# Kernel tuning notes

Measured on AMD Instinct MI355X. Metric: run time of the kernel, lower is better.

## Reference

```python
import jax, jax.numpy as jnp
import numpy as np

B, S, D, H, DK, DV = 4, 1024, 1024, 16, 64, 64
NEG = jnp.float32(-1e10)


def setup_inputs() -> dict:
    key = jax.random.key(0)
    ks = jax.random.split(key, 9)
    q = jax.random.normal(ks[0], (B, S, D), dtype=jnp.float32)
    k = jax.random.normal(ks[1], (B, S, D), dtype=jnp.float32)
    v = jax.random.normal(ks[2], (B, S, D), dtype=jnp.float32)
    pad_mask_1 = jax.random.randint(ks[3], (B,), 1, S + 1, dtype=jnp.int32)
    pad_mask_2 = jax.random.randint(ks[4], (B,), 1, S + 1, dtype=jnp.int32)
    # Per-head projection weights stacked over heads (torch Linear, bias=False).
    sc = 1.0 / np.sqrt(D)
    Wq = jax.random.uniform(ks[5], (H, D, DK), jnp.float32, -sc, sc)
    Wk = jax.random.uniform(ks[6], (H, D, DK), jnp.float32, -sc, sc)
    Wv = jax.random.uniform(ks[7], (H, D, DV), jnp.float32, -sc, sc)
    Wo = jax.random.uniform(ks[8], (H * DV, D), jnp.float32, -sc, sc)
    return {"q": q, "k": k, "v": v, "pad_mask_1": pad_mask_1,
            "pad_mask_2": pad_mask_2, "Wq": Wq, "Wk": Wk, "Wv": Wv, "Wo": Wo}


def reference(q, k, v, pad_mask_1, pad_mask_2, Wq, Wk, Wv, Wo):
    Bq, Sq, _ = q.shape
    scale = jnp.sqrt(jnp.float32(Wq.shape[-1]))
    qh = jnp.einsum('bsd,hdk->bhsk', q, Wq)   # [B,H,S,DK]
    kh = jnp.einsum('bsd,hdk->bhsk', k, Wk)
    vh = jnp.einsum('bsd,hdv->bhsv', v, Wv)
    w = jnp.einsum('bhqk,bhtk->bhqt', qh, kh) / scale  # [B,H,S,S]
    idx = jnp.arange(Sq)
    # pad_mask_1: mask key columns >= length; pad_mask_2: mask query rows >= length
    key_dead = idx[None, :] >= pad_mask_1[:, None]      # [B,S]
    row_dead = idx[None, :] >= pad_mask_2[:, None]      # [B,S]
    w = jnp.where(key_dead[:, None, None, :], NEG, w)
    w = jnp.where(row_dead[:, None, :, None], NEG, w)
    # causal: w.tril() + (-1e10).triu(1) == keep lower triangle, NEG strictly above
    causal = idx[None, :] > idx[:, None]                # [S,S] strictly upper
    w = jnp.where(causal[None, None], NEG, w)
    a = jax.nn.softmax(w, axis=-1)
    o = jnp.einsum('bhqt,bhtv->bhqv', a, vh)            # [B,H,S,DV]
    o = o.transpose(0, 2, 1, 3).reshape(Bq, Sq, -1)     # concat heads (head-major)
    return o @ Wo
```

## Files before the change

kernel.cpp:

```cpp
#include <hip/hip_runtime.h>

#define B_ 4
#define S_ 1024
#define D_ 1024
#define H_ 16
#define BSD (B_*S_*D_)

typedef unsigned short ushort_t;
typedef __attribute__((ext_vector_type(8))) __bf16 bf16x8;
typedef __attribute__((ext_vector_type(8))) ushort_t ushortx8;
typedef __attribute__((ext_vector_type(4))) float f32x4;

__device__ __forceinline__ ushort_t f2bf(float f) {
  union { float f; unsigned int u; } x; x.f = f;
  unsigned int r = x.u + 0x7fffu + ((x.u >> 16) & 1u);
  return (ushort_t)(r >> 16);
}

__device__ __forceinline__ void gll16(const void* g, void* l) {
  __builtin_amdgcn_global_load_lds(
      (const __attribute__((address_space(1))) unsigned int*)g,
      (__attribute__((address_space(3))) unsigned int*)l, 16, 0, 0);
}

__global__ __launch_bounds__(256) void transpose_w(
    const float* __restrict__ Wq, const float* __restrict__ Wk,
    const float* __restrict__ Wv, const float* __restrict__ Wo,
    ushort_t* __restrict__ WqT, ushort_t* __restrict__ WkT,
    ushort_t* __restrict__ WvT, ushort_t* __restrict__ WoT)
{
  __shared__ float tile[64][65];
  int blk = blockIdx.x;
  const float* src; ushort_t* dst;
  size_t sbase, dbase; int ld_src, ld_dst, r0, c0;
  if (blk < 768) {
    int tz = blk / 256;
    int rem = blk % 256; int head = rem >> 4; int kt = rem & 15;
    src = (tz == 0) ? Wq : (tz == 1) ? Wk : Wv;
    dst = (tz == 0) ? WqT : (tz == 1) ? WkT : WvT;
    sbase = (size_t)head * 1024 * 64; dbase = (size_t)head * 64 * 1024;
    ld_src = 64; ld_dst = 1024; r0 = kt * 64; c0 = 0;
  } else {
    int idx = blk - 768; src = Wo; dst = WoT;
    sbase = 0; dbase = 0; ld_src = 1024; ld_dst = 1024;
    r0 = (idx >> 4) * 64; c0 = (idx & 15) * 64;
  }
  int tid = threadIdx.x; int col = tid & 63; int rbase = tid >> 6;
  #pragma unroll
  for (int j = 0; j < 16; ++j) {
    int row = j * 4 + rbase;
    tile[row][col] = src[sbase + (size_t)(r0 + row) * ld_src + c0 + col];
  }
  __syncthreads();
  #pragma unroll
  for (int j = 0; j < 16; ++j) {
    int orow = j * 4 + rbase;
    dst[dbase + (size_t)(c0 + orow) * ld_dst + r0 + col] = f2bf(tile[col][orow]);
  }
}

__device__ __forceinline__ void gemm_body_f32A(
    const float* __restrict__ Af, const ushort_t* __restrict__ BT,
    ushort_t* __restrict__ Cb, int epi, int m0, int n0, int K)
{
  __shared__ __align__(16) ushort_t As[2][128 * 64];
  __shared__ __align__(16) ushort_t Bs[2][128 * 64];
  const int tid = threadIdx.x;
  const int wave = tid >> 6, lane = tid & 63;
  const int wm = wave >> 2, wn = wave & 3;

  f32x4 acc[4][2] = {};
  float4 areg[2][2];

  auto loadA = [&](int k0) {
    #pragma unroll
    for (int i = 0; i < 2; ++i) {
      int off = ((i * 8 + wave) << 10) + lane * 16;
      int row = off >> 7;
      int cb = off & 127;
      int lcb = cb ^ ((row & 7) << 4);
      const float* src = Af + (size_t)(m0 + row) * K + k0 + (lcb >> 1);
      areg[i][0] = *(const float4*)(src);
      areg[i][1] = *(const float4*)(src + 4);
    }
  };
  auto writeA = [&](int buf) {
    #pragma unroll
    for (int i = 0; i < 2; ++i) {
      int off = ((i * 8 + wave) << 10) + lane * 16;
      ushortx8 t;
      #pragma unroll
      for (int j = 0; j < 4; ++j) {
        t[j]     = f2bf(((const float*)&areg[i][0])[j]);
        t[4 + j] = f2bf(((const float*)&areg[i][1])[j]);
      }
      *(ushortx8*)((char*)As[buf] + off) = t;
    }
  };
  auto stageB = [&](int buf, int k0) {
    #pragma unroll
    for (int i = 0; i < 2; ++i) {
      int off = ((i * 8 + wave) << 10) + lane * 16;
      int row = off >> 7;
      int cb = off & 127;
      int lcb = cb ^ ((row & 7) << 4);
      gll16(BT + (size_t)(n0 + row) * K + k0 + (lcb >> 1), (char*)Bs[buf] + off);
    }
  };

  auto compute = [&](int buf) {
    #pragma unroll
    for (int kk = 0; kk < 2; ++kk) {
      bf16x8 af[4], bfr[2];
      #pragma unroll
      for (int mf = 0; mf < 4; ++mf) {
        int row = wm * 64 + mf * 16 + (lane & 15);
        int cb = kk * 64 + ((lane >> 4) << 4);
        af[mf] = *(const bf16x8*)((const char*)As[buf] + (row << 7) + (cb ^ ((row & 7) << 4)));
      }
      #pragma unroll
      for (int nf = 0; nf < 2; ++nf) {
        int row = wn * 32 + nf * 16 + (lane & 15);
        int cb = kk * 64 + ((lane >> 4) << 4);
        bfr[nf] = *(const bf16x8*)((const char*)Bs[buf] + (row << 7) + (cb ^ ((row & 7) << 4)));
      }
      #pragma unroll
      for (int mf = 0; mf < 4; ++mf)
        #pragma unroll
        for (int nf = 0; nf < 2; ++nf)
          acc[mf][nf] = __builtin_amdgcn_mfma_f32_16x16x32_bf16(af[mf], bfr[nf], acc[mf][nf], 0, 0, 0);
    }
  };

  const int nt = K >> 6;
  loadA(0);
  stageB(0, 0);
  writeA(0);
  __syncthreads();
  int cur = 0;
  for (int t = 0; t < nt - 1; ++t) {
    loadA((t + 1) << 6);
    stageB(cur ^ 1, (t + 1) << 6);
    compute(cur);
    writeA(cur ^ 1);
    __syncthreads();
    cur ^= 1;
  }
  compute(cur);

  #pragma unroll
  for (int mf = 0; mf < 4; ++mf) {
    #pragma unroll
    for (int nf = 0; nf < 2; ++nf) {
      #pragma unroll
      for (int r = 0; r < 4; ++r) {
        int m = m0 + wm * 64 + mf * 16 + ((lane >> 4) << 2) + r;
        int n = n0 + wn * 32 + nf * 16 + (lane & 15);
        float val = acc[mf][nf][r];
        if (epi == 0) {
          int b = m >> 10, s = m & 1023, h = n >> 6, dk = n & 63;
          Cb[((((size_t)(b * H_ + h)) << 10) + s) * 64 + dk] = f2bf(val);
        } else {
          int b = m >> 10, s = m & 1023, h = n >> 6, dv = n & 63;
          Cb[((((size_t)(b * H_ + h)) * 64 + dv) << 10) + s] = f2bf(val);
        }
      }
    }
  }
}

__device__ __forceinline__ void gemm_body(
    const ushort_t* __restrict__ A, const ushort_t* __restrict__ BT,
    float* __restrict__ Cf, int m0, int n0, int K)
{
  __shared__ __align__(16) ushort_t As[2][128 * 64];
  __shared__ __align__(16) ushort_t Bs[2][128 * 64];
  const int tid = threadIdx.x;
  const int wave = tid >> 6, lane = tid & 63;
  const int wm = wave >> 2, wn = wave & 3;

  f32x4 acc[4][2] = {};

  auto stage = [&](int buf, int k0) {
    #pragma unroll
    for (int i = 0; i < 2; ++i) {
      int off = ((i * 8 + wave) << 10) + lane * 16;
      int row = off >> 7;
      int cb = off & 127;
      int lcb = cb ^ ((row & 7) << 4);
      gll16(A + (size_t)(m0 + row) * K + k0 + (lcb >> 1), (char*)As[buf] + off);
      gll16(BT + (size_t)(n0 + row) * K + k0 + (lcb >> 1), (char*)Bs[buf] + off);
    }
  };

  auto compute = [&](int buf) {
    #pragma unroll
    for (int kk = 0; kk < 2; ++kk) {
      bf16x8 af[4], bfr[2];
      #pragma unroll
      for (int mf = 0; mf < 4; ++mf) {
        int row = wm * 64 + mf * 16 + (lane & 15);
        int cb = kk * 64 + ((lane >> 4) << 4);
        af[mf] = *(const bf16x8*)((const char*)As[buf] + (row << 7) + (cb ^ ((row & 7) << 4)));
      }
      #pragma unroll
      for (int nf = 0; nf < 2; ++nf) {
        int row = wn * 32 + nf * 16 + (lane & 15);
        int cb = kk * 64 + ((lane >> 4) << 4);
        bfr[nf] = *(const bf16x8*)((const char*)Bs[buf] + (row << 7) + (cb ^ ((row & 7) << 4)));
      }
      #pragma unroll
      for (int mf = 0; mf < 4; ++mf)
        #pragma unroll
        for (int nf = 0; nf < 2; ++nf)
          acc[mf][nf] = __builtin_amdgcn_mfma_f32_16x16x32_bf16(af[mf], bfr[nf], acc[mf][nf], 0, 0, 0);
    }
  };

  const int nt = K >> 6;
  stage(0, 0);
  __syncthreads();
  int cur = 0;
  for (int t = 0; t < nt - 1; ++t) {
    stage(cur ^ 1, (t + 1) << 6);
    compute(cur);
    __syncthreads();
    cur ^= 1;
  }
  compute(cur);

  #pragma unroll
  for (int mf = 0; mf < 4; ++mf) {
    #pragma unroll
    for (int nf = 0; nf < 2; ++nf) {
      #pragma unroll
      for (int r = 0; r < 4; ++r) {
        int m = m0 + wm * 64 + mf * 16 + ((lane >> 4) << 2) + r;
        int n = n0 + wn * 32 + nf * 16 + (lane & 15);
        Cf[(size_t)m * 1024 + n] = acc[mf][nf][r];
      }
    }
  }
}

__global__ __launch_bounds__(512, 4) void proj_gemm(
    const float* q, const float* k, const float* v,
    const ushort_t* WqT, const ushort_t* WkT, const ushort_t* WvT,
    ushort_t* qh, ushort_t* kh, ushort_t* vhT)
{
  int f = blockIdx.x;
  int xcd = f & 7;
  int slot = f >> 3;
  int g = xcd * 12 + (slot >> 3);
  int y = slot & 7;
  int z = g >> 5, x = g & 31;
  const float* A = (z == 0) ? q : (z == 1) ? k : v;
  const ushort_t* BT = (z == 0) ? WqT : (z == 1) ? WkT : WvT;
  ushort_t* C = (z == 0) ? qh : (z == 1) ? kh : vhT;
  gemm_body_f32A(A, BT, C, (z == 2) ? 1 : 0, x * 128, y * 128, 1024);
}

__global__ __launch_bounds__(512, 4) void out_gemm(
    const ushort_t* o, const ushort_t* WoT, float* out)
{
  int f = blockIdx.x;
  int xcd = f & 7;
  int slot = f >> 3;
  int x = xcd * 4 + (slot >> 3);
  int y = slot & 7;
  gemm_body(o, WoT, out, x * 128, y * 128, 1024);
}

__global__ __launch_bounds__(256) void meanv_kernel(
    const ushort_t* __restrict__ vhT, float* __restrict__ meanV)
{
  int row = blockIdx.x * 4 + (threadIdx.x >> 6);
  int lane = threadIdx.x & 63;
  const ushort_t* src = vhT + ((size_t)row << 10) + lane * 16;
  float s = 0.f;
  #pragma unroll
  for (int i = 0; i < 2; ++i) {
    bf16x8 v = *(const bf16x8*)(src + i * 8);
    #pragma unroll
    for (int j = 0; j < 8; ++j) s += (float)v[j];
  }
  #pragma unroll
  for (int mm = 1; mm < 64; mm <<= 1) s += __shfl_xor(s, mm);
  if (lane == 0) meanV[row] = s * (1.0f / 1024.0f);
}

__global__ __launch_bounds__(256) void attn_kernel(
    const ushort_t* __restrict__ qh, const ushort_t* __restrict__ kh,
    const ushort_t* __restrict__ vhT, const float* __restrict__ meanV,
    const int* __restrict__ pad1p, const int* __restrict__ pad2p,
    ushort_t* __restrict__ o)
{
  const int bh = blockIdx.x;
  const int b = bh >> 4, h = bh & 15;
  const int q0 = blockIdx.y << 6;
  const int pad1 = pad1p[b], pad2 = pad2p[b];
  const int tid = threadIdx.x, wave = tid >> 6, lane = tid & 63;

  if (q0 >= pad2) {
    int dv = tid & 63;
    int rw = tid >> 6;
    ushort_t mb = f2bf(meanV[(bh << 6) + dv]);
    for (int r = rw; r < 64; r += 4)
      o[(((size_t)((b << 10) + q0 + r)) << 10) + (h << 6) + dv] = mb;
    return;
  }

  __shared__ __align__(16) ushort_t Ks[64 * 64];
  __shared__ __align__(16) ushort_t Vs[64 * 64];
  __shared__ __align__(16) ushort_t Ps[4][16 * 64];

  const ushort_t* qbase = qh + ((size_t)bh << 16);
  const ushort_t* kbase = kh + ((size_t)bh << 16);
  const ushort_t* vbase = vhT + ((size_t)bh << 16);

  const int qrow = q0 + wave * 16 + (lane & 15);
  bf16x8 qf[2];
  qf[0] = *(const bf16x8*)(qbase + (size_t)qrow * 64 + ((lane >> 4) << 3));
  qf[1] = *(const bf16x8*)(qbase + (size_t)qrow * 64 + 32 + ((lane >> 4) << 3));

  f32x4 acc[4] = {};
  float mrow[4] = { -1e30f, -1e30f, -1e30f, -1e30f };
  float lrow[4] = { 0.f, 0.f, 0.f, 0.f };
  const int ribase = q0 + wave * 16 + ((lane >> 4) << 2);

  int t_hi = min(q0 + 63, min(pad2 - 1, pad1 - 1));
  int nb = (t_hi >> 6) + 1;

  for (int kb = 0; kb < nb; ++kb) {
    const int t0 = kb << 6;
    #pragma unroll
    for (int i = 0; i < 2; ++i) {
      int off = ((i * 4 + wave) << 10) + lane * 16;
      int row = off >> 7;
      int cb = off & 127;
      int lcb = cb ^ ((row & 7) << 4);
      gll16(kbase + (size_t)(t0 + row) * 64 + (lcb >> 1), (char*)Ks + off);
      gll16(vbase + ((size_t)row << 10) + t0 + (lcb >> 1), (char*)Vs + off);
    }
    __syncthreads();

    f32x4 sc[4];
    #pragma unroll
    for (int nf = 0; nf < 4; ++nf) {
      sc[nf] = (f32x4){0.f, 0.f, 0.f, 0.f};
      #pragma unroll
      for (int kk = 0; kk < 2; ++kk) {
        int trow = nf * 16 + (lane & 15);
        int cb = kk * 64 + ((lane >> 4) << 4);
        bf16x8 kf = *(const bf16x8*)((const char*)Ks + (trow << 7) + (cb ^ ((trow & 7) << 4)));
        sc[nf] = __builtin_amdgcn_mfma_f32_16x16x32_bf16(qf[kk], kf, sc[nf], 0, 0, 0);
      }
    }

    float pv[4][4];
    #pragma unroll
    for (int r = 0; r < 4; ++r) {
      const int irow = ribase + r;
      float sval[4];
      float rmax = -1e30f;
      #pragma unroll
      for (int nf = 0; nf < 4; ++nf) {
        int t = t0 + nf * 16 + (lane & 15);
        float vv = sc[nf][r] * 0.125f;
        if (t > irow || t >= pad1) vv = -1e10f;
        sval[nf] = vv;
        rmax = fmaxf(rmax, vv);
      }
      #pragma unroll
      for (int mm = 1; mm < 16; mm <<= 1) rmax = fmaxf(rmax, __shfl_xor(rmax, mm));
      float nm = fmaxf(mrow[r], rmax);
      float fscale = __expf(mrow[r] - nm);
      float rsum = 0.f;
      #pragma unroll
      for (int nf = 0; nf < 4; ++nf) {
        float p = __expf(sval[nf] - nm);
        pv[nf][r] = p;
        rsum += p;
      }
      #pragma unroll
      for (int mm = 1; mm < 16; mm <<= 1) rsum += __shfl_xor(rsum, mm);
      mrow[r] = nm;
      lrow[r] = lrow[r] * fscale + rsum;
      #pragma unroll
      for (int dvf = 0; dvf < 4; ++dvf) acc[dvf][r] *= fscale;
    }

    #pragma unroll
    for (int nf = 0; nf < 4; ++nf) {
      #pragma unroll
      for (int r = 0; r < 4; ++r) {
        int prow = ((lane >> 4) << 2) + r;
        int cbw = (nf * 16 + (lane & 15)) * 2;
        *(ushort_t*)((char*)Ps[wave] + (prow << 7) + (cbw ^ ((prow & 7) << 4))) = f2bf(pv[nf][r]);
      }
    }

    #pragma unroll
    for (int kk = 0; kk < 2; ++kk) {
      int prow = lane & 15;
      int cb = kk * 64 + ((lane >> 4) << 4);
      bf16x8 pf = *(const bf16x8*)((const char*)Ps[wave] + (prow << 7) + (cb ^ ((prow & 7) << 4)));
      #pragma unroll
      for (int dvf = 0; dvf < 4; ++dvf) {
        int vrow = dvf * 16 + (lane & 15);
        bf16x8 vfr = *(const bf16x8*)((const char*)Vs + (vrow << 7) + (cb ^ ((vrow & 7) << 4)));
        acc[dvf] = __builtin_amdgcn_mfma_f32_16x16x32_bf16(pf, vfr, acc[dvf], 0, 0, 0);
      }
    }
    __syncthreads();
  }

  #pragma unroll
  for (int dvf = 0; dvf < 4; ++dvf) {
    #pragma unroll
    for (int r = 0; r < 4; ++r) {
      int irow = ribase + r;
      int dv = dvf * 16 + (lane & 15);
      float val;
      if (irow < pad2) val = acc[dvf][r] * (1.0f / lrow[r]);
      else val = meanV[(bh << 6) + dv];
      o[(((size_t)((b << 10) + irow)) << 10) + (h << 6) + dv] = f2bf(val);
    }
  }
}

extern "C" void kernel_launch(void* const* d_in, const int* in_sizes, int n_in,
                              void* d_out, int out_size, void* d_ws, size_t ws_size,
                              hipStream_t stream) {
  (void)in_sizes; (void)n_in; (void)out_size; (void)ws_size;
  const float* q = (const float*)d_in[0];
  const float* k = (const float*)d_in[1];
  const float* v = (const float*)d_in[2];
  const int* pad1 = (const int*)d_in[3];
  const int* pad2 = (const int*)d_in[4];
  const float* Wq = (const float*)d_in[5];
  const float* Wk = (const float*)d_in[6];
  const float* Wv = (const float*)d_in[7];
  const float* Wo = (const float*)d_in[8];
  float* out = (float*)d_out;

  char* ws = (char*)d_ws;
  const size_t MB = 1u << 20;
  ushort_t* WqT = (ushort_t*)(ws + 24 * MB);
  ushort_t* WkT = (ushort_t*)(ws + 26 * MB);
  ushort_t* WvT = (ushort_t*)(ws + 28 * MB);
  ushort_t* WoT = (ushort_t*)(ws + 30 * MB);
  ushort_t* qh  = (ushort_t*)(ws + 32 * MB);
  ushort_t* kh  = (ushort_t*)(ws + 40 * MB);
  ushort_t* vhT = (ushort_t*)(ws + 48 * MB);
  ushort_t* ob  = (ushort_t*)(ws + 56 * MB);
  float* meanV  = (float*)(ws + 64 * MB);

  transpose_w<<<1024, 256, 0, stream>>>(Wq, Wk, Wv, Wo, WqT, WkT, WvT, WoT);
  proj_gemm<<<768, 512, 0, stream>>>(q, k, v, WqT, WkT, WvT, qh, kh, vhT);
  meanv_kernel<<<1024, 256, 0, stream>>>(vhT, meanV);
  attn_kernel<<<dim3(64, 16), 256, 0, stream>>>(qh, kh, vhT, meanV, pad1, pad2, ob);
  out_gemm<<<256, 512, 0, stream>>>(ob, WoT, out);
}
```

Baseline: 112.2 us.

## Prefetch A two tiles ahead with partial vmcnt waits in projection GEMM

```diff
diff --git a/kernel.cpp b/kernel.cpp
--- a/kernel.cpp
+++ b/kernel.cpp
@@ -70,9 +70,9 @@
   const int wm = wave >> 2, wn = wave & 3;
 
   f32x4 acc[4][2] = {};
-  float4 areg[2][2];
-
-  auto loadA = [&](int k0) {
+  float4 aA[2][2], aB[2][2];
+
+  auto loadA = [&](float4 (&dst)[2][2], int k0) {
     #pragma unroll
     for (int i = 0; i < 2; ++i) {
       int off = ((i * 8 + wave) << 10) + lane * 16;
@@ -80,21 +80,21 @@
       int cb = off & 127;
       int lcb = cb ^ ((row & 7) << 4);
       const float* src = Af + (size_t)(m0 + row) * K + k0 + (lcb >> 1);
-      areg[i][0] = *(const float4*)(src);
-      areg[i][1] = *(const float4*)(src + 4);
-    }
-  };
-  auto writeA = [&](int buf) {
+      dst[i][0] = *(const float4*)(src);
+      dst[i][1] = *(const float4*)(src + 4);
+    }
+  };
+  auto writeA = [&](int buf, const float4 (&src)[2][2]) {
     #pragma unroll
     for (int i = 0; i < 2; ++i) {
       int off = ((i * 8 + wave) << 10) + lane * 16;
-      ushortx8 t;
+      ushortx8 tv;
       #pragma unroll
       for (int j = 0; j < 4; ++j) {
-        t[j]     = f2bf(((const float*)&areg[i][0])[j]);
-        t[4 + j] = f2bf(((const float*)&areg[i][1])[j]);
-      }
-      *(ushortx8*)((char*)As[buf] + off) = t;
+        tv[j]     = f2bf(((const float*)&src[i][0])[j]);
+        tv[4 + j] = f2bf(((const float*)&src[i][1])[j]);
+      }
+      *(ushortx8*)((char*)As[buf] + off) = tv;
     }
   };
   auto stageB = [&](int buf, int k0) {
@@ -132,21 +132,39 @@
     }
   };
 
+#define CBAR4() do { asm volatile("s_waitcnt vmcnt(4) lgkmcnt(0)" ::: "memory"); \
+                     __builtin_amdgcn_s_barrier(); } while (0)
+
   const int nt = K >> 6;
-  loadA(0);
+  loadA(aA, 0);
   stageB(0, 0);
-  writeA(0);
-  __syncthreads();
-  int cur = 0;
-  for (int t = 0; t < nt - 1; ++t) {
-    loadA((t + 1) << 6);
-    stageB(cur ^ 1, (t + 1) << 6);
-    compute(cur);
-    writeA(cur ^ 1);
-    __syncthreads();
-    cur ^= 1;
-  }
-  compute(cur);
+  writeA(0, aA);
+  loadA(aA, 64);
+  CBAR4();
+
+  for (int t = 0; t < nt - 2; t += 2) {
+    stageB(1, (t + 1) << 6);
+    loadA(aB, (t + 2) << 6);
+    __builtin_amdgcn_sched_barrier(0);
+    compute(0);
+    writeA(1, aA);
+    CBAR4();
+    stageB(0, (t + 2) << 6);
+    loadA(aA, (t + 3) << 6);
+    __builtin_amdgcn_sched_barrier(0);
+    compute(1);
+    writeA(0, aB);
+    CBAR4();
+  }
+  stageB(1, (nt - 1) << 6);
+  __builtin_amdgcn_sched_barrier(0);
+  compute(0);
+  writeA(1, aA);
+  asm volatile("s_waitcnt vmcnt(0) lgkmcnt(0)" ::: "memory");
+  __builtin_amdgcn_s_barrier();
+  compute(1);
+
+#undef CBAR4
 
   #pragma unroll
   for (int mf = 0; mf < 4; ++mf) {
```

Result: faster. 108.7 us (-3.2%).
